# Kernel tuning notes

Hardware: AMD Instinct MI355X
Metric: run time of the kernel (lower is better)

Reference implementation:

```python
import jax, jax.numpy as jnp
import numpy as np
from jax import lax

B = 2048; T = 16; K = 12; G = T * B; NODES = G * (K + 1)
ENC = 64; GIN = 32; GHID = 64; GOUT = 32; EMB = 32; DEMB = 16
DYN = 32; DEC = 128; TOUT = 25; GRID = (13, 3); SCONV = 64; C31 = 16
SOC = ((GRID[0] - 4 + 1) // 2) * C31  # 80
TE = EMB * 3 + DEMB + GOUT            # 144


def _lstm(xs, Wih, Whh, bih, bhh):
    # xs: (T, N, in) seq-first, torch LSTM gate order i,f,g,o
    n = xs.shape[1]; H = Whh.shape[1]
    def step(carry, x):
        h, c = carry
        g = x @ Wih.T + h @ Whh.T + bih + bhh
        i, f, gg, o = jnp.split(g, 4, axis=-1)
        c = jax.nn.sigmoid(f) * c + jax.nn.sigmoid(i) * jnp.tanh(gg)
        h = jax.nn.sigmoid(o) * jnp.tanh(c)
        return (h, c), h
    z = jnp.zeros((n, H), xs.dtype)
    (h, _), hs = lax.scan(step, (z, z), xs)
    return hs, h


def _gat(x, src, dst, W, a_s, a_d, b, n):
    # PyG GATConv, heads=1, self-loops already in src/dst, leaky slope 0.2
    xw = x @ W.T
    e = jax.nn.leaky_relu((xw @ a_s)[src] + (xw @ a_d)[dst], 0.2)
    m = jax.ops.segment_max(e, dst, num_segments=n)
    ex = jnp.exp(e - m[dst])
    den = jax.ops.segment_sum(ex, dst, num_segments=n)
    alpha = ex / den[dst]
    return jax.ops.segment_sum(xw[src] * alpha[:, None], dst, num_segments=n) + b


def setup_inputs() -> dict:
    key = jax.random.key(0)
    ks = iter(jax.random.split(key, 80))
    f = lambda *s: jax.random.normal(next(ks), s, jnp.float32) * 0.05
    base = np.arange(G, dtype=np.int32) * (K + 1)          # ego node of each group
    nb = (base[:, None] + 1 + np.arange(K, dtype=np.int32)).reshape(-1)
    ego = np.repeat(base, K)
    edge_index = jnp.asarray(np.stack([np.concatenate([nb, ego]), np.concatenate([ego, nb])]))
    batch_gat = jnp.asarray(np.repeat(np.arange(G, dtype=np.int32), K + 1))
    m = np.zeros((B, GRID[1] * GRID[0], ENC), bool); m[:, :K, :] = True
    masks = jnp.asarray(m.reshape(B, GRID[1], GRID[0], ENC))
    return dict(
        data_figure_x=f(NODES, 4), edge_index=edge_index, batch_gat=batch_gat,
        hist=f(T, B, 2), hist_va=f(T, B, 2), hist_dis=f(T, B, 1), hist_lane=f(T, B, 2),
        nbrs=f(T, B * K, 2), nbrs_va=f(T, B * K, 2), nbrs_dis=f(T, B * K, 1), nbrs_lane=f(T, B * K, 2),
        masks=masks, lat_enc=f(B, 3), lon_enc=f(B, 2),
        ip_emb_W=f(GIN, 4), ip_emb_b=f(GIN),
        gat1_W=f(GHID, GIN), gat1_as=f(GHID), gat1_ad=f(GHID), gat1_b=f(GHID),
        gat2_W=f(GOUT, GHID), gat2_as=f(GOUT), gat2_ad=f(GOUT), gat2_b=f(GOUT),
        pos_W=f(EMB, 2), pos_b=f(EMB), va_W=f(EMB, 2), va_b=f(EMB),
        dis_W=f(DEMB, 1), dis_b=f(DEMB), lane_W=f(EMB, 2), lane_b=f(EMB),
        enc_Wih=f(4 * ENC, TE), enc_Whh=f(4 * ENC, ENC), enc_bih=f(4 * ENC), enc_bhh=f(4 * ENC),
        ta_Wih=f(4 * ENC, TE), ta_Whh=f(4 * ENC, ENC), ta_bih=f(4 * ENC), ta_bhh=f(4 * ENC),
        ta_TA_W=f(T, T * ENC), ta_TA_b=f(T),
        dyn_W=f(DYN, ENC), dyn_b=f(DYN),
        sconv_W=f(SCONV, ENC, 3, 3), sconv_b=f(SCONV),
        conv31_W=f(C31, SCONV, 3, 1), conv31_b=f(C31),
        dec_Wih=f(4 * DEC, 2 * SOC + DYN + 5), dec_Whh=f(4 * DEC, DEC), dec_bih=f(4 * DEC), dec_bhh=f(4 * DEC),
        op_W=f(5, DEC), op_b=f(5),
        oplat_W=f(3, 2 * SOC + DYN), oplat_b=f(3), oplon_W=f(2, 2 * SOC + DYN), oplon_b=f(2))


def reference(data_figure_x, edge_index, batch_gat, hist, hist_va, hist_dis, hist_lane,
              nbrs, nbrs_va, nbrs_dis, nbrs_lane, masks, lat_enc, lon_enc,
              ip_emb_W, ip_emb_b, gat1_W, gat1_as, gat1_ad, gat1_b,
              gat2_W, gat2_as, gat2_ad, gat2_b,
              pos_W, pos_b, va_W, va_b, dis_W, dis_b, lane_W, lane_b,
              enc_Wih, enc_Whh, enc_bih, enc_bhh,
              ta_Wih, ta_Whh, ta_bih, ta_bhh, ta_TA_W, ta_TA_b,
              dyn_W, dyn_b, sconv_W, sconv_b, conv31_W, conv31_b,
              dec_Wih, dec_Whh, dec_bih, dec_bhh, op_W, op_b,
              oplat_W, oplat_b, oplon_W, oplon_b):
    n = data_figure_x.shape[0]
    lrelu = lambda x: jax.nn.leaky_relu(x, 0.1)
    loop = jnp.arange(n, dtype=edge_index.dtype)
    src = jnp.concatenate([edge_index[0], loop])
    dst = jnp.concatenate([edge_index[1], loop])
    h = lrelu(data_figure_x @ ip_emb_W.T + ip_emb_b)
    h = lrelu(_gat(h, src, dst, gat1_W, gat1_as, gat1_ad, gat1_b, n))
    h = lrelu(_gat(h, src, dst, gat2_W, gat2_as, gat2_ad, gat2_b, n))
    # first node per group -> ego (hist), rest -> neighbors (batch_gat sorted)
    first_idx = jnp.searchsorted(batch_gat, jnp.arange(G, dtype=batch_gat.dtype))
    hist_gat = h[first_idx].reshape(T, B, GOUT)          # dropout = eval identity
    nbr_mask = jnp.ones(n, bool).at[first_idx].set(False)
    nbr_idx = jnp.where(nbr_mask, size=n - G)[0]
    nbrs_gat = h[nbr_idx].reshape(T, -1, GOUT)
    emb = lambda x, W, b: lrelu(x @ W.T + b)
    ch = jnp.concatenate([emb(hist, pos_W, pos_b), emb(hist_va, va_W, va_b),
                          emb(hist_dis, dis_W, dis_b), emb(hist_lane, lane_W, lane_b), hist_gat], -1)
    cn = jnp.concatenate([emb(nbrs, pos_W, pos_b), emb(nbrs_va, va_W, va_b),
                          emb(nbrs_dis, dis_W, dis_b), emb(nbrs_lane, lane_W, lane_b), nbrs_gat], -1)
    # TA_LSTM: temporal attention over per-step hidden states
    hs, _ = _lstm(ch, ta_Wih, ta_Whh, ta_bih, ta_bhh)     # (T, B, ENC)
    total = hs.transpose(1, 0, 2).reshape(B, T * ENC)
    beta = jax.nn.softmax(jax.nn.relu(total @ ta_TA_W.T + ta_TA_b), axis=-1)
    hist_enc = lrelu(jnp.einsum('tbh,bt->bh', hs, beta) @ dyn_W.T + dyn_b)
    _, nbrs_enc = _lstm(cn, enc_Wih, enc_Whh, enc_bih, enc_bhh)   # (B*K, ENC)
    # masked_scatter_: fill True positions row-major with flattened nbrs_enc
    mflat = masks.reshape(-1)
    sidx = jnp.clip(jnp.cumsum(mflat) - 1, 0)
    soc = jnp.where(mflat, nbrs_enc.reshape(-1)[sidx], 0.0).reshape(masks.shape).astype(jnp.float32)
    soc = soc.transpose(0, 3, 2, 1)                       # (B, ENC, 13, 3)
    dn = ('NCHW', 'OIHW', 'NCHW')
    soc = lrelu(lax.conv_general_dilated(soc, sconv_W, (1, 1), 'VALID', dimension_numbers=dn)
                + sconv_b[None, :, None, None])
    soc = lrelu(lax.conv_general_dilated(soc, conv31_W, (1, 1), 'VALID', dimension_numbers=dn)
                + conv31_b[None, :, None, None])          # (B, C31, 9, 1)
    pad = ((0, 0), (0, 0), (1, 1), (0, 0))
    mx = lax.reduce_window(soc, -jnp.inf, lax.max, (1, 1, 2, 1), (1, 1, 2, 1), pad).reshape(-1, SOC)
    av = (lax.reduce_window(soc, 0.0, lax.add, (1, 1, 2, 1), (1, 1, 2, 1), pad) / 2.0).reshape(-1, SOC)
    enc = jnp.concatenate([mx, av, hist_enc], 1)          # (B, 2*SOC+DYN)
    lat_pred = jax.nn.softmax(enc @ oplat_W.T + oplat_b, axis=1)
    lon_pred = jax.nn.softmax(enc @ oplon_W.T + oplon_b, axis=1)
    encd = jnp.concatenate([enc, lat_enc, lon_enc], 1)
    rep = jnp.broadcast_to(encd[None], (TOUT,) + encd.shape)
    hs2, _ = _lstm(rep, dec_Wih, dec_Whh, dec_bih, dec_bhh)
    fut = hs2 @ op_W.T + op_b                             # (TOUT, B, 5)
    out = jnp.concatenate([fut[..., 0:2], jnp.exp(fut[..., 2:4]), jnp.tanh(fut[..., 4:5])], -1)
    return out, lat_pred, lon_pred
```

## Files before the change

### kernel.cpp

```cpp
#include <hip/hip_runtime.h>
#include <hip/hip_bf16.h>
#include <cstddef>
#include <cstdint>
#include <math.h>

typedef __hip_bfloat16 bf16;
typedef _Float16 f16;
typedef _Float16 f16x8 __attribute__((ext_vector_type(8)));
typedef _Float16 f16x2 __attribute__((ext_vector_type(2)));
typedef float f32x4 __attribute__((ext_vector_type(4)));
#define MFMA16(a,b,c) __builtin_amdgcn_mfma_f32_16x16x32_f16(a,b,c,0,0,0)

#define DEV __device__ __forceinline__
DEV float bff(bf16 x){ return __bfloat162float(x); }
DEV bf16 fbf(float x){ return __float2bfloat16(x); }
DEV float lr01(float x){ return x>0.f? x : 0.1f*x; }
DEV float lr02(float x){ return x>0.f? x : 0.2f*x; }
DEV float frcp(float x){ return __builtin_amdgcn_rcpf(x); }
DEV float sigm(float x){ return frcp(1.f+__expf(-x)); }
DEV float tanhe(float x){ float a=fabsf(x); float e=__expf(-2.f*a); float t=(1.f-e)*frcp(1.f+e); return x<0.f? -t : t; }
DEV void stout(void* out, int isf, size_t i, float v){
  if (isf) ((float*)out)[i] = v; else ((bf16*)out)[i] = fbf(v);
}
DEV float bfu_lo(unsigned u){ return __uint_as_float(u << 16); }
DEV float bfu_hi(unsigned u){ return __uint_as_float(u & 0xffff0000u); }

#define NBATCH 2048
#define TSEQ 16
#define KNB 12
#define NGRP 32768
#define NNODES 425984
#define NBK 24576
#define NTOUT 25

__global__ __launch_bounds__(256) void detect_k(const uint32_t* __restrict__ x, int* __restrict__ flag) {
  __shared__ int cnt;
  if (threadIdx.x == 0) cnt = 0;
  __syncthreads();
  float v = __uint_as_float(x[threadIdx.x]);
  float a = fabsf(v);
  if (a > 1e-12f && a < 100.f) atomicAdd(&cnt, 1);
  __syncthreads();
  if (threadIdx.x == 0) *flag = (cnt >= 128) ? 1 : 0;
}

#define NCVT 55
struct CvtArgs {
  const void* src[NCVT];
  unsigned off[NCVT];
  unsigned cnt[NCVT];
};

__global__ __launch_bounds__(256) void cvt_k(CvtArgs a, float* __restrict__ dst,
                                             const int* __restrict__ flag, unsigned total) {
  const int isf = *flag;
  for (size_t e = (size_t)blockIdx.x*256 + threadIdx.x; e < total; e += (size_t)gridDim.x*256) {
    int lo = 0, hi = NCVT-1;
    while (lo < hi) { int mid = (lo+hi+1)>>1; if ((size_t)a.off[mid] <= e) lo = mid; else hi = mid-1; }
    unsigned r = (unsigned)(e - a.off[lo]);
    float v = isf ? ((const float*)a.src[lo])[r] : bff(((const bf16*)a.src[lo])[r]);
    dst[e] = v;
  }
}

__global__ __launch_bounds__(256) void prep_k(
    const float* __restrict__ scW, const float* __restrict__ c31W,
    const float* __restrict__ g1W, const float* __restrict__ g2W,
    const float* __restrict__ encWhh, const float* __restrict__ taWhh,
    const float* __restrict__ decWhh,
    f16* __restrict__ wp1t, f16* __restrict__ wp2t,
    float* __restrict__ w1t, float* __restrict__ w2t,
    f16* __restrict__ wench, f16* __restrict__ wtah, f16* __restrict__ wdech) {
  int idx = blockIdx.x*256 + threadIdx.x;
  if (idx < 12288) {
    int o = idx & 63; int k = idx >> 6; int kh = k >> 6; int i = k & 63;
    wp1t[idx] = (f16)scW[((size_t)(o*64+i)*3 + kh)*3];
  } else if (idx < 15360) {
    int e = idx - 12288;
    int o = e & 15; int k = e >> 4; int kh = k >> 6; int i = k & 63;
    wp2t[e] = (f16)c31W[(size_t)(o*64+i)*3 + kh];
  } else if (idx < 17408) {
    int e = idx - 15360; int k = e >> 6, f = e & 63;
    w1t[e] = g1W[f*32 + k];
  } else if (idx < 19456) {
    int e = idx - 17408; int k = e >> 5, f = e & 31;
    w2t[e] = g2W[f*64 + k];
  } else if (idx < 35840) {
    int e = idx - 19456;
    wench[e] = (f16)encWhh[e];
  } else if (idx < 52224) {
    int e = idx - 35840;
    wtah[e] = (f16)taWhh[e];
  } else if (idx < 117760) {
    int e = idx - 52224;
    wdech[e] = (f16)decWhh[e];
  }
}

__global__ __launch_bounds__(256) void gat_dense1_k(const float* __restrict__ x,
    const float* __restrict__ ipW, const float* __restrict__ ipb,
    const float* __restrict__ Wt, const float* __restrict__ as_, const float* __restrict__ ad_,
    bf16* __restrict__ out, float* __restrict__ esed) {
  __shared__ float As[64][33];
  __shared__ float Ws[32][64];
  __shared__ float xs[64][4];
  __shared__ float wipw[128];
  __shared__ float wipb[32];
  const int tid = threadIdx.x;
  const size_t bm = (size_t)blockIdx.x * 64;
  ((float*)xs)[tid] = x[bm*4 + tid];
  if (tid < 128) wipw[tid] = ipW[tid];
  else if (tid < 160) wipb[tid-128] = ipb[tid-128];
  #pragma unroll
  for (int i = 0; i < 8; i++) ((float*)Ws)[tid + 256*i] = Wt[tid + 256*i];
  __syncthreads();
  #pragma unroll
  for (int i = 0; i < 8; i++) {
    int e = tid + 256*i; int v = e >> 5, f = e & 31;
    float a = wipb[f];
    #pragma unroll
    for (int k = 0; k < 4; k++) a += xs[v][k]*wipw[f*4+k];
    As[v][f] = lr01(a);
  }
  __syncthreads();
  const int v = tid >> 2, f0 = (tid & 3) * 16;
  float acc[16];
  #pragma unroll
  for (int i = 0; i < 16; i++) acc[i] = 0.f;
  #pragma unroll 8
  for (int k = 0; k < 32; k++) {
    float a = As[v][k];
    const float4* wr = (const float4*)&Ws[k][f0];
    #pragma unroll
    for (int q = 0; q < 4; q++) {
      float4 w4 = wr[q];
      acc[4*q+0] += a*w4.x; acc[4*q+1] += a*w4.y; acc[4*q+2] += a*w4.z; acc[4*q+3] += a*w4.w;
    }
  }
  bf16* op = out + (bm+v)*64 + f0;
  #pragma unroll
  for (int i = 0; i < 16; i++) op[i] = fbf(acc[i]);
  float es = 0.f, ed = 0.f;
  #pragma unroll
  for (int i = 0; i < 16; i++) { es += acc[i]*as_[f0+i]; ed += acc[i]*ad_[f0+i]; }
  es += __shfl_xor(es, 1); es += __shfl_xor(es, 2);
  ed += __shfl_xor(ed, 1); ed += __shfl_xor(ed, 2);
  if ((tid & 3) == 0) { esed[(bm+v)*2] = es; esed[(bm+v)*2+1] = ed; }
}

__global__ __launch_bounds__(256) void gat_dense2_k(const bf16* __restrict__ in,
    const float* __restrict__ Wt, const float* __restrict__ as_, const float* __restrict__ ad_,
    bf16* __restrict__ out, float* __restrict__ esed) {
  __shared__ float As[64][65];
  __shared__ float Ws[64][32];
  const int tid = threadIdx.x;
  const size_t bm = (size_t)blockIdx.x * 64;
  #pragma unroll
  for (int i = 0; i < 16; i++) {
    int lin = tid + 256*i;
    As[lin>>6][lin&63] = bff(in[bm*64 + lin]);
    if (i < 8) ((float*)Ws)[tid + 256*i] = Wt[tid + 256*i];
  }
  __syncthreads();
  const int v = tid >> 2, f0 = (tid & 3) * 8;
  float acc[8];
  #pragma unroll
  for (int i = 0; i < 8; i++) acc[i] = 0.f;
  #pragma unroll 8
  for (int k = 0; k < 64; k++) {
    float a = As[v][k];
    const float4* wr = (const float4*)&Ws[k][f0];
    #pragma unroll
    for (int q = 0; q < 2; q++) {
      float4 w4 = wr[q];
      acc[4*q+0] += a*w4.x; acc[4*q+1] += a*w4.y; acc[4*q+2] += a*w4.z; acc[4*q+3] += a*w4.w;
    }
  }
  bf16* op = out + (bm+v)*32 + f0;
  #pragma unroll
  for (int i = 0; i < 8; i++) op[i] = fbf(acc[i]);
  float es = 0.f, ed = 0.f;
  #pragma unroll
  for (int i = 0; i < 8; i++) { es += acc[i]*as_[f0+i]; ed += acc[i]*ad_[f0+i]; }
  es += __shfl_xor(es, 1); es += __shfl_xor(es, 2);
  ed += __shfl_xor(ed, 1); ed += __shfl_xor(ed, 2);
  if ((tid & 3) == 0) { esed[(bm+v)*2] = es; esed[(bm+v)*2+1] = ed; }
}

__global__ __launch_bounds__(256) void alpha_k(const float* __restrict__ esed, float* __restrict__ alph) {
  int g = blockIdx.x*256 + threadIdx.x;
  size_t base = (size_t)g*13;
  float esv[13], edv[13];
  #pragma unroll
  for (int i = 0; i < 13; i++) { esv[i] = esed[(base+i)*2]; edv[i] = esed[(base+i)*2+1]; }
  float* o = alph + (size_t)g*40;
  float e[13]; float m = -1e30f;
  #pragma unroll
  for (int i = 0; i < 13; i++) { float z = lr02(esv[i] + edv[0]); e[i] = z; m = fmaxf(m, z); }
  float den = 0.f;
  #pragma unroll
  for (int i = 0; i < 13; i++) { e[i] = __expf(e[i]-m); den += e[i]; }
  float inv = 1.f/den;
  #pragma unroll
  for (int i = 0; i < 13; i++) o[i] = e[i]*inv;
  #pragma unroll
  for (int j = 1; j <= 12; j++) {
    float z0 = lr02(esv[0] + edv[j]);
    float z1 = lr02(esv[j] + edv[j]);
    float mm = fmaxf(z0, z1);
    float a0 = __expf(z0-mm), a1 = __expf(z1-mm);
    float s = 1.f/(a0+a1);
    o[13 + 2*(j-1)] = a0*s;
    o[14 + 2*(j-1)] = a1*s;
  }
}

template<int F>
__global__ __launch_bounds__(256) void agg8_k(const bf16* __restrict__ xw, const float* __restrict__ alph,
                                              const float* __restrict__ bias, bf16* __restrict__ out) {
  const int NV = F/8;
  size_t idx = (size_t)blockIdx.x*256 + threadIdx.x;
  int f8 = (int)(idx % NV);
  size_t vn = idx / NV;
  int node = (int)(vn % 13);
  size_t g = vn / 13;
  size_t base = g*13;
  const float* al = alph + g*40;
  const int f0 = f8*8;
  float acc[8];
  if (node == 0) {
    #pragma unroll
    for (int j = 0; j < 8; j++) acc[j] = 0.f;
    #pragma unroll
    for (int i = 0; i < 13; i++) {
      const uint4 rv = *(const uint4*)&xw[(base+i)*F + f0];
      float a = al[i];
      acc[0] += a*bfu_lo(rv.x); acc[1] += a*bfu_hi(rv.x);
      acc[2] += a*bfu_lo(rv.y); acc[3] += a*bfu_hi(rv.y);
      acc[4] += a*bfu_lo(rv.z); acc[5] += a*bfu_hi(rv.z);
      acc[6] += a*bfu_lo(rv.w); acc[7] += a*bfu_hi(rv.w);
    }
  } else {
    float a0 = al[13 + 2*(node-1)], a1 = al[14 + 2*(node-1)];
    const uint4 r0v = *(const uint4*)&xw[base*F + f0];
    const uint4 r1v = *(const uint4*)&xw[(base+node)*F + f0];
    acc[0] = a0*bfu_lo(r0v.x) + a1*bfu_lo(r1v.x);
    acc[1] = a0*bfu_hi(r0v.x) + a1*bfu_hi(r1v.x);
    acc[2] = a0*bfu_lo(r0v.y) + a1*bfu_lo(r1v.y);
    acc[3] = a0*bfu_hi(r0v.y) + a1*bfu_hi(r1v.y);
    acc[4] = a0*bfu_lo(r0v.z) + a1*bfu_lo(r1v.z);
    acc[5] = a0*bfu_hi(r0v.z) + a1*bfu_hi(r1v.z);
    acc[6] = a0*bfu_lo(r0v.w) + a1*bfu_lo(r1v.w);
    acc[7] = a0*bfu_hi(r0v.w) + a1*bfu_hi(r1v.w);
  }
  bf16* op = out + vn*F + f0;
  #pragma unroll
  for (int j = 0; j < 8; j++) op[j] = fbf(lr01(acc[j] + bias[f0+j]));
}

template<bool NBR>
__global__ __launch_bounds__(256) void gemm_embed_mfma_k(
    const float* __restrict__ p_in, const float* __restrict__ v_in,
    const float* __restrict__ di_in, const float* __restrict__ l_in,
    const bf16* __restrict__ h2,
    const float* __restrict__ posW, const float* __restrict__ posb,
    const float* __restrict__ vaW, const float* __restrict__ vab,
    const float* __restrict__ disW, const float* __restrict__ disb,
    const float* __restrict__ laneW, const float* __restrict__ laneb,
    const float* __restrict__ W, f16* __restrict__ C, int t0) {
  __shared__ __align__(16) f16 As[128][40];
  __shared__ __align__(16) f16 Bs[128][40];
  const int tid = threadIdx.x;
  const int bm = blockIdx.x * 128, bn = blockIdx.y * 128;
  const int bz = blockIdx.z;
  const int mm = tid & 127, par = tid >> 7;
  int t, n2;
  if (NBR) { t = t0 + bz; n2 = bm + mm; }
  else { int gm = bm + mm; t = gm >> 11; n2 = gm & 2047; }
  const int NROW = NBR ? NBK : NBATCH;
  size_t rn = (size_t)t*NROW + n2;
  const float px0 = p_in[rn*2], px1 = p_in[rn*2+1];
  const float vx0 = v_in[rn*2], vx1 = v_in[rn*2+1];
  const float dx  = di_in[rn];
  const float lx0 = l_in[rn*2], lx1 = l_in[rn*2+1];
  const int b = NBR ? (n2 / KNB) : n2;
  const int node_off = NBR ? (1 + n2 % KNB) : 0;
  const bf16* h2p = h2 + (((size_t)t*NBATCH + b)*13 + node_off)*32;
  const int wn = bn + mm;
  const int l = tid & 63, wv = tid >> 6;
  const int lr = l & 15, lq = l >> 4;
  f32x4 acc[2][8];
  #pragma unroll
  for (int rt = 0; rt < 2; rt++)
    #pragma unroll
    for (int ct = 0; ct < 8; ct++) acc[rt][ct] = (f32x4){0.f,0.f,0.f,0.f};
  for (int ks = 0; ks < 5; ks++) {
    const int k0 = ks*32;
    #pragma unroll
    for (int e = 0; e < 16; e++) {
      int kk = par + 2*e;
      int f = k0 + kk;
      float val;
      if (f < 32) {
        val = lr01(px0*posW[f*2] + px1*posW[f*2+1] + posb[f]);
      } else if (f < 64) {
        int ff = f-32;
        val = lr01(vx0*vaW[ff*2] + vx1*vaW[ff*2+1] + vab[ff]);
      } else if (f < 80) {
        int ff = f-64;
        val = lr01(dx*disW[ff] + disb[ff]);
      } else if (f < 112) {
        int ff = f-80;
        val = lr01(lx0*laneW[ff*2] + lx1*laneW[ff*2+1] + laneb[ff]);
      } else if (f < 144) {
        val = bff(h2p[f-112]);
      } else val = 0.f;
      As[mm][kk] = (f16)val;
      Bs[mm][kk] = (f < 144) ? (f16)W[(size_t)wn*144 + f] : (f16)0.f;
    }
    __syncthreads();
    f16x8 a0 = *(const f16x8*)&As[wv*32 + lr][lq*8];
    f16x8 a1 = *(const f16x8*)&As[wv*32 + 16 + lr][lq*8];
    #pragma unroll
    for (int ct = 0; ct < 8; ct++) {
      f16x8 bfr = *(const f16x8*)&Bs[ct*16 + lr][lq*8];
      acc[0][ct] = MFMA16(a0, bfr, acc[0][ct]);
      acc[1][ct] = MFMA16(a1, bfr, acc[1][ct]);
    }
    __syncthreads();
  }
  #pragma unroll
  for (int rt = 0; rt < 2; rt++)
    #pragma unroll
    for (int ct = 0; ct < 8; ct++)
      #pragma unroll
      for (int rg = 0; rg < 4; rg++) {
        int row = wv*32 + rt*16 + lq*4 + rg;
        int col = ct*16 + lr;
        size_t orow = NBR ? ((size_t)bz*NBK + bm + row) : (size_t)(bm + row);
        C[orow*256 + bn + col] = (f16)acc[rt][ct][rg];
      }
}

__global__ __launch_bounds__(512, 4) void enc_ta_mega_k(
    const float* __restrict__ p_in, const float* __restrict__ v_in,
    const float* __restrict__ di_in, const float* __restrict__ l_in,
    const bf16* __restrict__ h2,
    const float* __restrict__ posW, const float* __restrict__ posb,
    const float* __restrict__ vaW, const float* __restrict__ vab,
    const float* __restrict__ disW, const float* __restrict__ disb,
    const float* __restrict__ laneW, const float* __restrict__ laneb,
    const float* __restrict__ Wih, const f16* __restrict__ Whh16,
    const float* __restrict__ bih, const float* __restrict__ bhh,
    float* __restrict__ hstate,
    const f16* __restrict__ XWta, const f16* __restrict__ Whh16ta,
    const float* __restrict__ bihta, const float* __restrict__ bhhta,
    float* __restrict__ h_all_ta) {
  __shared__ __align__(16) union SMem {
    struct { f16 As_s[2][16][168]; f16 h_s[2][16][72]; float gates[16][258]; } e;
    struct { f16 h_s[16][72]; float gates[16][260]; } a;
  } sm;
  const int tid = threadIdx.x;
  const int l = tid & 63;
  const int lr = l & 15, lq = l >> 4;

  if (blockIdx.x < 128) {
    const int r0 = blockIdx.x * 16;
    const int wv = tid >> 6;
    const int u = l, rg = wv;
    f16x8 bf[4][2];
    if (wv < 4) {
      #pragma unroll
      for (int ct = 0; ct < 4; ct++)
        #pragma unroll
        for (int kt = 0; kt < 2; kt++)
          bf[ct][kt] = *(const f16x8*)&Whh16ta[(size_t)(wv*64 + ct*16 + lr)*64 + kt*32 + lq*8];
    }
    float bj4[4];
    #pragma unroll
    for (int g = 0; g < 4; g++) bj4[g] = bihta[g*64+u] + bhhta[g*64+u];
    for (int i = tid; i < 16*64; i += 512) sm.a.h_s[i>>6][i&63] = (f16)0.f;
    float c[4] = {0.f,0.f,0.f,0.f};
    __syncthreads();
    #pragma unroll 1
    for (int s = 0; s < TSEQ; s++) {
      if (wv < 4) {
        f16x8 a0 = *(const f16x8*)&sm.a.h_s[lr][lq*8];
        f16x8 a1 = *(const f16x8*)&sm.a.h_s[lr][32 + lq*8];
        f32x4 acc[4];
        #pragma unroll
        for (int ct = 0; ct < 4; ct++) {
          acc[ct] = (f32x4){0.f,0.f,0.f,0.f};
          acc[ct] = MFMA16(a0, bf[ct][0], acc[ct]);
          acc[ct] = MFMA16(a1, bf[ct][1], acc[ct]);
        }
        #pragma unroll
        for (int ct = 0; ct < 4; ct++)
          #pragma unroll
          for (int q2 = 0; q2 < 4; q2++)
            sm.a.gates[lq*4 + q2][wv*64 + ct*16 + lr] = acc[ct][q2];
      }
      __syncthreads();
      if (wv < 4) {
        const f16* xwrow = XWta + ((size_t)s*NBATCH + r0)*256;
        #pragma unroll
        for (int q = 0; q < 4; q++) {
          const int r = rg*4 + q;
          float gi = sm.a.gates[r][u]     + bj4[0] + (float)xwrow[(size_t)r*256 + u];
          float gf = sm.a.gates[r][64+u]  + bj4[1] + (float)xwrow[(size_t)r*256 + 64 + u];
          float gg = sm.a.gates[r][128+u] + bj4[2] + (float)xwrow[(size_t)r*256 + 128 + u];
          float go = sm.a.gates[r][192+u] + bj4[3] + (float)xwrow[(size_t)r*256 + 192 + u];
          float cv = sigm(gf)*c[q] + sigm(gi)*tanhe(gg);
          c[q] = cv;
          float hv = sigm(go)*tanhe(cv);
          sm.a.h_s[r][u] = (f16)hv;
          h_all_ta[((size_t)s*NBATCH + r0 + r)*64 + u] = hv;
        }
      }
      __syncthreads();
    }
    return;
  }

  const int r0 = (blockIdx.x - 128) * 16;
  const int w = tid >> 6;
  const int cu0 = w*16 + lr;
  const int cu1 = 128 + cu0;
  f16x8 bxw[2][5];
  f16x8 bhw[2][2];
  float bv[2];
  #pragma unroll
  for (int s = 0; s < 2; s++) {
    const int cu = s ? cu1 : cu0;
    const float* wr = Wih + (size_t)cu*144;
    #pragma unroll
    for (int ks = 0; ks < 5; ks++) {
      f16x8 v;
      #pragma unroll
      for (int j = 0; j < 8; j++) {
        int k = ks*32 + lq*8 + j;
        v[j] = (k < 144) ? (f16)wr[k] : (f16)0.f;
      }
      bxw[s][ks] = v;
    }
    #pragma unroll
    for (int kt = 0; kt < 2; kt++)
      bhw[s][kt] = *(const f16x8*)&Whh16[(size_t)cu*64 + kt*32 + lq*8];
    bv[s] = bih[cu] + bhh[cu];
  }
  const int prow = tid & 15;
  const int pq = tid >> 4;
  const int n2 = r0 + prow;
  const int bb = n2 / KNB;
  const int noff = 1 + n2 - bb*KNB;
  float c0 = 0.f, c1 = 0.f;
  float La = 0.f, Lb = 0.f;
  uint4 HA = {0,0,0,0};
  for (int i = tid; i < 16*64; i += 512) sm.e.h_s[0][i>>6][i&63] = (f16)0.f;

#define ENC_ISSUE(TP) do {                                                   \
    const size_t rnp = (size_t)(TP)*NBK + n2;                                \
    if (pq < 4)       { float2 p = *(const float2*)(p_in + rnp*2); La = p.x; Lb = p.y; } \
    else if (pq < 8)  { float2 p = *(const float2*)(v_in + rnp*2); La = p.x; Lb = p.y; } \
    else if (pq < 10) { La = di_in[rnp]; }                                   \
    else if (pq < 14) { float2 p = *(const float2*)(l_in + rnp*2); La = p.x; Lb = p.y; } \
    else if (pq < 18) { HA = *(const uint4*)(h2 + (((size_t)(TP)*NBATCH + bb)*13 + noff)*32 + (pq-14)*8); } \
  } while (0)

#define ENC_STAGE(BUF) do {                                                  \
    if (pq < 20) {                                                           \
      const int f0 = pq*8;                                                   \
      f16x8 v;                                                               \
      if (f0 < 32) {                                                         \
        _Pragma("unroll")                                                    \
        for (int j = 0; j < 8; j++)                                          \
          v[j] = (f16)lr01(La*posW[(f0+j)*2] + Lb*posW[(f0+j)*2+1] + posb[f0+j]); \
      } else if (f0 < 64) {                                                  \
        _Pragma("unroll")                                                    \
        for (int j = 0; j < 8; j++) {                                        \
          int ff = f0+j-32;                                                  \
          v[j] = (f16)lr01(La*vaW[ff*2] + Lb*vaW[ff*2+1] + vab[ff]);         \
        }                                                                    \
      } else if (f0 < 80) {                                                  \
        _Pragma("unroll")                                                    \
        for (int j = 0; j < 8; j++) {                                        \
          int ff = f0+j-64;                                                  \
          v[j] = (f16)lr01(La*disW[ff] + disb[ff]);                          \
        }                                                                    \
      } else if (f0 < 112) {                                                 \
        _Pragma("unroll")                                                    \
        for (int j = 0; j < 8; j++) {                                        \
          int ff = f0+j-80;                                                  \
          v[j] = (f16)lr01(La*laneW[ff*2] + Lb*laneW[ff*2+1] + laneb[ff]);   \
        }                                                                    \
      } else if (f0 < 144) {                                                 \
        v[0] = (f16)bfu_lo(HA.x); v[1] = (f16)bfu_hi(HA.x);                  \
        v[2] = (f16)bfu_lo(HA.y); v[3] = (f16)bfu_hi(HA.y);                  \
        v[4] = (f16)bfu_lo(HA.z); v[5] = (f16)bfu_hi(HA.z);                  \
        v[6] = (f16)bfu_lo(HA.w); v[7] = (f16)bfu_hi(HA.w);                  \
      } else {                                                               \
        _Pragma("unroll")                                                    \
        for (int j = 0; j < 8; j++) v[j] = (f16)0.f;                         \
      }                                                                      \
      *(f16x8*)&sm.e.As_s[BUF][prow][f0] = v;                                \
    }                                                                        \
  } while (0)

  ENC_ISSUE(0);
  ENC_STAGE(0);
  __syncthreads();
  int cur = 0;
  #pragma unroll 1
  for (int t = 0; t < TSEQ; t++) {
    const int tp = (t+1 < TSEQ) ? t+1 : t;
    ENC_ISSUE(tp);
    {
      f16x8 ae0 = *(const f16x8*)&sm.e.As_s[cur][lr][lq*8];
      f16x8 ae1 = *(const f16x8*)&sm.e.As_s[cur][lr][32 + lq*8];
      f16x8 ae2 = *(const f16x8*)&sm.e.As_s[cur][lr][64 + lq*8];
      f16x8 ae3 = *(const f16x8*)&sm.e.As_s[cur][lr][96 + lq*8];
      f16x8 ae4 = *(const f16x8*)&sm.e.As_s[cur][lr][128 + lq*8];
      f16x8 ah0 = *(const f16x8*)&sm.e.h_s[cur][lr][lq*8];
      f16x8 ah1 = *(const f16x8*)&sm.e.h_s[cur][lr][32 + lq*8];
      #pragma unroll
      for (int s = 0; s < 2; s++) {
        f32x4 a = (f32x4){0.f,0.f,0.f,0.f};
        a = MFMA16(ae0, bxw[s][0], a);
        a = MFMA16(ae1, bxw[s][1], a);
        a = MFMA16(ae2, bxw[s][2], a);
        a = MFMA16(ae3, bxw[s][3], a);
        a = MFMA16(ae4, bxw[s][4], a);
        a = MFMA16(ah0, bhw[s][0], a);
        a = MFMA16(ah1, bhw[s][1], a);
        const int cu = s ? cu1 : cu0;
        #pragma unroll
        for (int q = 0; q < 4; q++)
          sm.e.gates[lq*4 + q][cu] = a[q] + bv[s];
      }
    }
    __syncthreads();
    {
      const int u0 = pq*2;
      const float* gr = &sm.e.gates[prow][0];
      float gi0 = gr[u0],       gi1 = gr[u0+1];
      float gf0 = gr[64+u0],    gf1 = gr[64+u0+1];
      float gg0 = gr[128+u0],   gg1 = gr[128+u0+1];
      float go0 = gr[192+u0],   go1 = gr[192+u0+1];
      float cv0 = sigm(gf0)*c0 + sigm(gi0)*tanhe(gg0);
      float cv1 = sigm(gf1)*c1 + sigm(gi1)*tanhe(gg1);
      c0 = cv0; c1 = cv1;
      f16x2 hv;
      hv[0] = (f16)(sigm(go0)*tanhe(cv0));
      hv[1] = (f16)(sigm(go1)*tanhe(cv1));
      *(f16x2*)&sm.e.h_s[cur^1][prow][u0] = hv;
    }
    ENC_STAGE(cur^1);
    __syncthreads();
    cur ^= 1;
  }
#undef ENC_ISSUE
#undef ENC_STAGE
  for (int i = tid; i < 16*64; i += 512)
    hstate[(size_t)(r0 + (i>>6))*64 + (i&63)] = (float)sm.e.h_s[cur][i>>6][i&63];
}

__global__ __launch_bounds__(256, 2) void gemm_bt(const bf16* __restrict__ A, const float* __restrict__ W,
                                                  float* __restrict__ C, int M, int N, int Kd) {
  __shared__ __align__(16) float As[8][132];
  __shared__ __align__(16) float Bs[8][132];
  const int tid = threadIdx.x;
  const int bm = blockIdx.x * 128, bn = blockIdx.y * 128;
  const int tx = tid & 15, ty = tid >> 4;
  float acc[8][8];
  #pragma unroll
  for (int i = 0; i < 8; i++)
    #pragma unroll
    for (int j = 0; j < 8; j++) acc[i][j] = 0.f;
  for (int k0 = 0; k0 < Kd; k0 += 8) {
    #pragma unroll
    for (int i = 0; i < 4; i++) {
      int lin = tid + 256*i;
      int kk = lin & 7, mm = lin >> 3;
      int gk = k0 + kk;
      As[kk][mm] = (gk < Kd) ? bff(A[(size_t)(bm+mm)*Kd + gk]) : 0.f;
      Bs[kk][mm] = (gk < Kd) ? W[(size_t)(bn+mm)*Kd + gk] : 0.f;
    }
    __syncthreads();
    #pragma unroll
    for (int kk = 0; kk < 8; kk++) {
      float4 a0 = *(const float4*)&As[kk][ty*4];
      float4 a1 = *(const float4*)&As[kk][64+ty*4];
      float4 b0 = *(const float4*)&Bs[kk][tx*4];
      float4 b1 = *(const float4*)&Bs[kk][64+tx*4];
      float av[8] = {a0.x,a0.y,a0.z,a0.w,a1.x,a1.y,a1.z,a1.w};
      float bv[8] = {b0.x,b0.y,b0.z,b0.w,b1.x,b1.y,b1.z,b1.w};
      #pragma unroll
      for (int i = 0; i < 8; i++)
        #pragma unroll
        for (int j = 0; j < 8; j++) acc[i][j] += av[i]*bv[j];
    }
    __syncthreads();
  }
  #pragma unroll
  for (int i = 0; i < 8; i++) {
    int m = bm + (i>>2)*64 + ty*4 + (i&3);
    #pragma unroll
    for (int jh = 0; jh < 2; jh++) {
      float4 v = make_float4(acc[i][jh*4+0], acc[i][jh*4+1], acc[i][jh*4+2], acc[i][jh*4+3]);
      *(float4*)&C[(size_t)m*N + bn + jh*64 + tx*4] = v;
    }
  }
}

__global__ __launch_bounds__(512) void lstm128_mfma_k(const float* __restrict__ XW,
    const f16* __restrict__ Whh16, const float* __restrict__ bih, const float* __restrict__ bhh,
    int steps, float* __restrict__ h_all) {
  __shared__ __align__(16) f16 h_s[2][16][136];
  const int tid = threadIdx.x;
  const int r0 = blockIdx.x * 16;
  const int l = tid & 63, wv = tid >> 6;
  const int lr = l & 15, lq = l >> 4;
  const int u = wv*16 + lr;
  f16x8 bf[4][4];
  #pragma unroll
  for (int g = 0; g < 4; g++)
    #pragma unroll
    for (int kt = 0; kt < 4; kt++)
      bf[g][kt] = *(const f16x8*)&Whh16[(size_t)(g*128 + u)*128 + kt*32 + lq*8];
  float xr[4][4];
  #pragma unroll
  for (int g = 0; g < 4; g++) {
    float bj = bih[g*128 + u] + bhh[g*128 + u];
    #pragma unroll
    for (int rg = 0; rg < 4; rg++)
      xr[g][rg] = XW[(size_t)(r0 + lq*4 + rg)*512 + g*128 + u] + bj;
  }
  for (int i = tid; i < 16*128; i += 512) h_s[0][i>>7][i&127] = (f16)0.f;
  float c[4] = {0.f,0.f,0.f,0.f};
  __syncthreads();
  int cur = 0;
  for (int t = 0; t < steps; t++) {
    f16x8 a0 = *(const f16x8*)&h_s[cur][lr][lq*8];
    f16x8 a1 = *(const f16x8*)&h_s[cur][lr][32 + lq*8];
    f16x8 a2 = *(const f16x8*)&h_s[cur][lr][64 + lq*8];
    f16x8 a3 = *(const f16x8*)&h_s[cur][lr][96 + lq*8];
    f32x4 acc[4];
    #pragma unroll
    for (int g = 0; g < 4; g++) {
      acc[g] = (f32x4){0.f,0.f,0.f,0.f};
      acc[g] = MFMA16(a0, bf[g][0], acc[g]);
      acc[g] = MFMA16(a1, bf[g][1], acc[g]);
      acc[g] = MFMA16(a2, bf[g][2], acc[g]);
      acc[g] = MFMA16(a3, bf[g][3], acc[g]);
    }
    #pragma unroll
    for (int rg = 0; rg < 4; rg++) {
      const int row = lq*4 + rg;
      float gi = acc[0][rg] + xr[0][rg];
      float gf = acc[1][rg] + xr[1][rg];
      float gg = acc[2][rg] + xr[2][rg];
      float go = acc[3][rg] + xr[3][rg];
      float cv = sigm(gf)*c[rg] + sigm(gi)*tanhe(gg);
      c[rg] = cv;
      float hv = sigm(go)*tanhe(cv);
      h_s[cur^1][row][u] = (f16)hv;
      h_all[((size_t)t*NBATCH + r0 + row)*128 + u] = hv;
    }
    __syncthreads();
    cur ^= 1;
  }
}

__global__ __launch_bounds__(256) void ta_fused_k(const float* __restrict__ hs,
    const float* __restrict__ W, const float* __restrict__ bias,
    const float* __restrict__ dynW, const float* __restrict__ dynb,
    float* __restrict__ henc) {
  __shared__ float hsl[8][1024];
  __shared__ float scl[8][16];
  const int tid = threadIdx.x;
  const int b0 = blockIdx.x * 8;
  for (int i = tid; i < 8*1024; i += 256) {
    int bb = i >> 10, r = i & 1023;
    int t = r >> 6, h = r & 63;
    hsl[bb][r] = hs[((size_t)t*NBATCH + b0 + bb)*64 + h];
  }
  __syncthreads();
  if (tid < 128) {
    int bb = tid >> 4, i = tid & 15;
    float acc = bias[i];
    for (int t = 0; t < 16; t++) {
      const float* hr = &hsl[bb][t*64];
      const float* wr = W + (size_t)i*1024 + t*64;
      #pragma unroll
      for (int h = 0; h < 64; h++) acc += hr[h]*wr[h];
    }
    scl[bb][i] = fmaxf(acc, 0.f);
  }
  __syncthreads();
  {
    int bb = tid >> 5, o = tid & 31;
    const float* s = scl[bb];
    float m = s[0];
    #pragma unroll
    for (int t = 1; t < 16; t++) m = fmaxf(m, s[t]);
    float e[16]; float den = 0.f;
    #pragma unroll
    for (int t = 0; t < 16; t++) { e[t] = __expf(s[t]-m); den += e[t]; }
    float inv = 1.f/den;
    float acc = dynb[o];
    for (int t = 0; t < 16; t++) {
      const float* hr = &hsl[bb][t*64];
      float inner = 0.f;
      #pragma unroll
      for (int h = 0; h < 64; h++) inner += hr[h]*dynW[(size_t)o*64 + h];
      acc += (e[t]*inv)*inner;
    }
    henc[(size_t)(b0+bb)*32 + o] = lr01(acc);
  }
}

__global__ __launch_bounds__(256) void fused_conv_k(const float* __restrict__ nenc,
    const f16* __restrict__ wp1t, const f16* __restrict__ wp2t,
    const float* __restrict__ scb, const float* __restrict__ c31b,
    const float* __restrict__ henc, const float* __restrict__ lat_enc, const float* __restrict__ lon_enc,
    float* __restrict__ e192, bf16* __restrict__ encd) {
  __shared__ f16 ws1[12288];
  __shared__ f16 ws2[3072];
  __shared__ float img[4][13][64];
  __shared__ float c1s[4][64][12];
  __shared__ float c2s[4][16][9];
  const int tid = threadIdx.x;
  const int l = tid & 63, wv = tid >> 6;
  const int b = blockIdx.x*4 + wv;
  #pragma unroll
  for (int it = 0; it < 24; it++) ((uint32_t*)ws1)[tid + 256*it] = ((const uint32_t*)wp1t)[tid + 256*it];
  #pragma unroll
  for (int it = 0; it < 6; it++) ((uint32_t*)ws2)[tid + 256*it] = ((const uint32_t*)wp2t)[tid + 256*it];
  #pragma unroll
  for (int it = 0; it < 13; it++)
    img[wv][it][l] = (it < 12) ? nenc[((size_t)b*12 + it)*64 + l] : 0.f;
  __syncthreads();
  {
    const int o = l;
    float acc[11];
    float bv = scb[o];
    #pragma unroll
    for (int h = 0; h < 11; h++) acc[h] = bv;
    for (int k = 0; k < 192; k++) {
      int kh = k >> 6, i = k & 63;
      float w = (float)ws1[k*64 + o];
      const float* ic = img[wv][kh];
      #pragma unroll
      for (int h = 0; h < 11; h++) acc[h] += ic[h*64 + i] * w;
    }
    #pragma unroll
    for (int h = 0; h < 11; h++) c1s[wv][o][h] = lr01(acc[h]);
  }
  __syncthreads();
  if (l < 48) {
    const int o2 = l / 3, jg = l - o2*3;
    float acc[3];
    float bv = c31b[o2];
    #pragma unroll
    for (int m = 0; m < 3; m++) acc[m] = bv;
    for (int k = 0; k < 192; k++) {
      int kh = k >> 6, i = k & 63;
      float w = (float)ws2[k*16 + o2];
      #pragma unroll
      for (int m = 0; m < 3; m++) acc[m] += c1s[wv][i][jg*3 + m + kh] * w;
    }
    #pragma unroll
    for (int m = 0; m < 3; m++) c2s[wv][o2][jg*3 + m] = lr01(acc[m]);
  }
  __syncthreads();
  for (int it = 0; it < 4; it++) {
    int k = l + it*64;
    if (k >= 197) break;
    float val;
    if (k < 192) {
      if (k < 160) {
        bool is_av = (k >= 80);
        int rel = is_av ? (k - 80) : k;
        int o = rel / 5, p = rel - o*5;
        const float* r = c2s[wv][o];
        float v2 = r[2*p];
        if (p == 0) val = is_av ? v2*0.5f : v2;
        else { float v1 = r[2*p-1]; val = is_av ? (v1+v2)*0.5f : fmaxf(v1, v2); }
      } else {
        val = henc[(size_t)b*32 + (k-160)];
      }
      e192[(size_t)b*192 + k] = val;
    } else if (k < 195) {
      val = lat_enc[(size_t)b*3 + (k-192)];
    } else {
      val = lon_enc[(size_t)b*2 + (k-195)];
    }
    encd[(size_t)b*197 + k] = fbf(val);
  }
}

__global__ __launch_bounds__(256) void latlon_k(const float* __restrict__ e192,
    const float* __restrict__ latW, const float* __restrict__ latb,
    const float* __restrict__ lonW, const float* __restrict__ lonb,
    void* __restrict__ out, const int* __restrict__ flag) {
  int b = blockIdx.x*256 + threadIdx.x;
  const int isf = *flag;
  const float* e = e192 + (size_t)b*192;
  float s[3];
  #pragma unroll
  for (int c2 = 0; c2 < 3; c2++) {
    float acc = latb[c2];
    for (int k = 0; k < 192; k++) acc += e[k]*latW[c2*192+k];
    s[c2] = acc;
  }
  float m = fmaxf(s[0], fmaxf(s[1], s[2]));
  float e0 = __expf(s[0]-m), e1 = __expf(s[1]-m), e2 = __expf(s[2]-m);
  float inv = 1.f/(e0+e1+e2);
  stout(out, isf, 256000 + (size_t)b*3 + 0, e0*inv);
  stout(out, isf, 256000 + (size_t)b*3 + 1, e1*inv);
  stout(out, isf, 256000 + (size_t)b*3 + 2, e2*inv);
  float q[2];
  #pragma unroll
  for (int c2 = 0; c2 < 2; c2++) {
    float acc = lonb[c2];
    for (int k = 0; k < 192; k++) acc += e[k]*lonW[c2*192+k];
    q[c2] = acc;
  }
  float m2 = fmaxf(q[0], q[1]);
  float f0 = __expf(q[0]-m2), f1 = __expf(q[1]-m2);
  float inv2 = 1.f/(f0+f1);
  stout(out, isf, 262144 + (size_t)b*2 + 0, f0*inv2);
  stout(out, isf, 262144 + (size_t)b*2 + 1, f1*inv2);
}

__global__ __launch_bounds__(256) void out_k(const float* __restrict__ hs2, const float* __restrict__ opW,
                                             const float* __restrict__ opb,
                                             void* __restrict__ out, const int* __restrict__ flag) {
  int idx = blockIdx.x*256 + threadIdx.x;
  const int isf = *flag;
  const float* h = hs2 + (size_t)idx*128;
  float f[5];
  #pragma unroll
  for (int c2 = 0; c2 < 5; c2++) {
    float acc = opb[c2];
    #pragma unroll
    for (int k = 0; k < 128; k++) acc += h[k]*opW[c2*128+k];
    f[c2] = acc;
  }
  stout(out, isf, (size_t)idx*5 + 0, f[0]);
  stout(out, isf, (size_t)idx*5 + 1, f[1]);
  stout(out, isf, (size_t)idx*5 + 2, __expf(f[2]));
  stout(out, isf, (size_t)idx*5 + 3, __expf(f[3]));
  stout(out, isf, (size_t)idx*5 + 4, tanhe(f[4]));
}

static const size_t OFF_H2   = 0;
static const size_t OFF_P    = 6815744;
static const size_t OFF_Q    = 20447232;
static const size_t OFF_ESED = 34078720;
static const size_t OFF_ALPH = 34930688;
static const size_t OFF_XWTA = 6815744;
static const size_t OFF_HSTA = 15204352;
static const size_t OFF_SCO  = 17301504;
static const size_t OFF_HS2  = 6815744;
static const size_t OFF_HST  = 23691264;
static const size_t OFF_CST  = 25264128;
static const size_t OFF_E192 = 28573696;
static const size_t OFF_ENCD = 28966912;
static const size_t OFF_XWD  = 29168640;
static const size_t OFF_HEN  = 35000000;
static const size_t OFF_CVT  = 36241408;
static const size_t OFF_WP1T = 41280000;
static const size_t OFF_WP2T = 41286144;
static const size_t OFF_W1T  = 41287680;
static const size_t OFF_W2T  = 41289728;
static const size_t OFF_WENC = 41291776;
static const size_t OFF_WTAH = 41299968;
static const size_t OFF_WDECH= 41308160;
static const size_t OFF_FLAG = 41400000;

extern "C" void kernel_launch(void* const* d_in, const int* in_sizes, int n_in,
                              void* d_out, int out_size, void* d_ws, size_t ws_size,
                              hipStream_t stream) {
  (void)in_sizes; (void)n_in; (void)out_size; (void)ws_size;
  float* ws = (float*)d_ws;
  int* flag = (int*)(ws + OFF_FLAG);

  static const int   cidx[NCVT] = {0,3,4,5,6,7,8,9,10,12,13,
    14,15,16,17,18,19,20,21,22,23,24,25,26,27,28,29,30,31,
    32,33,34,35,36,37,38,39,40,41,42,43,44,45,46,47,
    48,49,50,51,52,53,54,55,56,57};
  static const unsigned ccnt[NCVT] = {1703936,65536,65536,32768,65536,786432,786432,393216,786432,6144,4096,
    128,32,2048,64,64,64,2048,32,32,32,64,32,64,32,16,16,64,32,
    36864,16384,256,256,36864,16384,256,256,16384,16,2048,32,36864,64,3072,16,
    100864,65536,512,512,640,5,576,3,384,2};
  CvtArgs ca;
  unsigned total = 0;
  float* cp[58];
  for (int i = 0; i < NCVT; i++) {
    ca.src[i] = d_in[cidx[i]];
    ca.off[i] = total;
    ca.cnt[i] = ccnt[i];
    cp[cidx[i]] = ws + OFF_CVT + total;
    total += ccnt[i];
  }
  detect_k<<<1,256,0,stream>>>((const uint32_t*)d_in[0], flag);
  cvt_k<<<4096,256,0,stream>>>(ca, ws + OFF_CVT, flag, total);

  void* out = d_out;
  bf16*  h2    = (bf16*)(ws + OFF_H2);
  bf16*  h1    = (bf16*)(ws + OFF_P);
  bf16*  xw1   = (bf16*)(ws + OFF_Q);
  bf16*  xw2   = (bf16*)(ws + OFF_Q);
  float* esed  = ws + OFF_ESED;
  float* alph  = ws + OFF_ALPH;
  f16*   xwta  = (f16*)(ws + OFF_XWTA);
  float* hsta  = ws + OFF_HSTA;
  float* henc  = ws + OFF_HEN;
  float* hst   = ws + OFF_HST;
  float* e192  = ws + OFF_E192;
  bf16*  encd  = (bf16*)(ws + OFF_ENCD);
  float* xwd   = ws + OFF_XWD;
  f16*   wp1t  = (f16*)(ws + OFF_WP1T);
  f16*   wp2t  = (f16*)(ws + OFF_WP2T);
  float* w1t   = ws + OFF_W1T;
  float* w2t   = ws + OFF_W2T;
  f16*   wench = (f16*)(ws + OFF_WENC);
  f16*   wtah  = (f16*)(ws + OFF_WTAH);
  f16*   wdech = (f16*)(ws + OFF_WDECH);
  float* hs2   = ws + OFF_HS2;

  prep_k<<<460,256,0,stream>>>(cp[44], cp[46], cp[16], cp[20], cp[33], cp[37], cp[49],
                               wp1t, wp2t, w1t, w2t, wench, wtah, wdech);

  gat_dense1_k<<<6656,256,0,stream>>>(cp[0], cp[14], cp[15], w1t, cp[17], cp[18], xw1, esed);
  alpha_k<<<128,256,0,stream>>>(esed, alph);
  agg8_k<64><<<13312,256,0,stream>>>(xw1, alph, cp[19], h1);
  gat_dense2_k<<<6656,256,0,stream>>>(h1, w2t, cp[21], cp[22], xw2, esed);
  alpha_k<<<128,256,0,stream>>>(esed, alph);
  agg8_k<32><<<6656,256,0,stream>>>(xw2, alph, cp[23], h2);

  gemm_embed_mfma_k<false><<<dim3(256,2,1),256,0,stream>>>(cp[3], cp[4], cp[5], cp[6], h2,
      cp[24],cp[25],cp[26],cp[27],cp[28],cp[29],cp[30],cp[31], cp[36], xwta, 0);

  enc_ta_mega_k<<<1664,512,0,stream>>>(cp[7], cp[8], cp[9], cp[10], h2,
      cp[24],cp[25],cp[26],cp[27],cp[28],cp[29],cp[30],cp[31],
      cp[32], wench, cp[34], cp[35], hst,
      xwta, wtah, cp[38], cp[39], hsta);

  ta_fused_k<<<256,256,0,stream>>>(hsta, cp[40], cp[41], cp[42], cp[43], henc);

  fused_conv_k<<<512,256,0,stream>>>(hst, wp1t, wp2t, cp[45], cp[47], henc, cp[12], cp[13], e192, encd);

  latlon_k<<<8,256,0,stream>>>(e192, cp[54], cp[55], cp[56], cp[57], out, flag);
  gemm_bt<<<dim3(16,4),256,0,stream>>>(encd, cp[48], xwd, NBATCH, 512, 197);
  lstm128_mfma_k<<<128,512,0,stream>>>(xwd, wdech, cp[50], cp[51], NTOUT, hs2);
  out_k<<<200,256,0,stream>>>(hs2, cp[52], cp[53], out, flag);
}
```

Measured before the change: 737.7 us.

## Fuse latlon head into decoder GEMM and output projection into decoder LSTM

Merges the lat/lon softmax kernel into the decoder input GEMM launch, with extra blocks handling the heads. It also folds the 5-wide output projection into the decoder LSTM loop, using an fp32 shared-memory copy of h instead of writing the full hidden history to global memory. This removes two kernel launches and the hs2 round trip to global memory. The cost is 80 threads doing a serial 128-length dot product each step inside the recurrent loop, which lengthens the critical path per step.

```diff
diff --git a/kernel.cpp b/kernel.cpp
--- a/kernel.cpp
+++ b/kernel.cpp
@@ -564,63 +564,103 @@
     hstate[(size_t)(r0 + (i>>6))*64 + (i&63)] = (float)sm.e.h_s[cur][i>>6][i&63];
 }
 
-__global__ __launch_bounds__(256, 2) void gemm_bt(const bf16* __restrict__ A, const float* __restrict__ W,
-                                                  float* __restrict__ C, int M, int N, int Kd) {
-  __shared__ __align__(16) float As[8][132];
-  __shared__ __align__(16) float Bs[8][132];
+__global__ __launch_bounds__(256, 2) void head_k(const bf16* __restrict__ A, const float* __restrict__ W,
+    float* __restrict__ C, int N, int Kd,
+    const float* __restrict__ e192,
+    const float* __restrict__ latW, const float* __restrict__ latb,
+    const float* __restrict__ lonW, const float* __restrict__ lonb,
+    void* __restrict__ out, const int* __restrict__ flag) {
   const int tid = threadIdx.x;
-  const int bm = blockIdx.x * 128, bn = blockIdx.y * 128;
-  const int tx = tid & 15, ty = tid >> 4;
-  float acc[8][8];
-  #pragma unroll
-  for (int i = 0; i < 8; i++)
-    #pragma unroll
-    for (int j = 0; j < 8; j++) acc[i][j] = 0.f;
-  for (int k0 = 0; k0 < Kd; k0 += 8) {
-    #pragma unroll
-    for (int i = 0; i < 4; i++) {
-      int lin = tid + 256*i;
-      int kk = lin & 7, mm = lin >> 3;
-      int gk = k0 + kk;
-      As[kk][mm] = (gk < Kd) ? bff(A[(size_t)(bm+mm)*Kd + gk]) : 0.f;
-      Bs[kk][mm] = (gk < Kd) ? W[(size_t)(bn+mm)*Kd + gk] : 0.f;
-    }
-    __syncthreads();
-    #pragma unroll
-    for (int kk = 0; kk < 8; kk++) {
-      float4 a0 = *(const float4*)&As[kk][ty*4];
-      float4 a1 = *(const float4*)&As[kk][64+ty*4];
-      float4 b0 = *(const float4*)&Bs[kk][tx*4];
-      float4 b1 = *(const float4*)&Bs[kk][64+tx*4];
-      float av[8] = {a0.x,a0.y,a0.z,a0.w,a1.x,a1.y,a1.z,a1.w};
-      float bv[8] = {b0.x,b0.y,b0.z,b0.w,b1.x,b1.y,b1.z,b1.w};
-      #pragma unroll
-      for (int i = 0; i < 8; i++)
+  if (blockIdx.x < 64) {
+    __shared__ __align__(16) float As[8][132];
+    __shared__ __align__(16) float Bs[8][132];
+    const int bm = (blockIdx.x >> 2) * 128, bn = (blockIdx.x & 3) * 128;
+    const int tx = tid & 15, ty = tid >> 4;
+    float acc[8][8];
+    #pragma unroll
+    for (int i = 0; i < 8; i++)
+      #pragma unroll
+      for (int j = 0; j < 8; j++) acc[i][j] = 0.f;
+    for (int k0 = 0; k0 < Kd; k0 += 8) {
+      #pragma unroll
+      for (int i = 0; i < 4; i++) {
+        int lin = tid + 256*i;
+        int kk = lin & 7, mm = lin >> 3;
+        int gk = k0 + kk;
+        As[kk][mm] = (gk < Kd) ? bff(A[(size_t)(bm+mm)*Kd + gk]) : 0.f;
+        Bs[kk][mm] = (gk < Kd) ? W[(size_t)(bn+mm)*Kd + gk] : 0.f;
+      }
+      __syncthreads();
+      #pragma unroll
+      for (int kk = 0; kk < 8; kk++) {
+        float4 a0 = *(const float4*)&As[kk][ty*4];
+        float4 a1 = *(const float4*)&As[kk][64+ty*4];
+        float4 b0 = *(const float4*)&Bs[kk][tx*4];
+        float4 b1 = *(const float4*)&Bs[kk][64+tx*4];
+        float av[8] = {a0.x,a0.y,a0.z,a0.w,a1.x,a1.y,a1.z,a1.w};
+        float bvv[8] = {b0.x,b0.y,b0.z,b0.w,b1.x,b1.y,b1.z,b1.w};
         #pragma unroll
-        for (int j = 0; j < 8; j++) acc[i][j] += av[i]*bv[j];
-    }
-    __syncthreads();
-  }
-  #pragma unroll
-  for (int i = 0; i < 8; i++) {
-    int m = bm + (i>>2)*64 + ty*4 + (i&3);
-    #pragma unroll
-    for (int jh = 0; jh < 2; jh++) {
-      float4 v = make_float4(acc[i][jh*4+0], acc[i][jh*4+1], acc[i][jh*4+2], acc[i][jh*4+3]);
-      *(float4*)&C[(size_t)m*N + bn + jh*64 + tx*4] = v;
-    }
-  }
-}
-
-__global__ __launch_bounds__(512) void lstm128_mfma_k(const float* __restrict__ XW,
+        for (int i = 0; i < 8; i++)
+          #pragma unroll
+          for (int j = 0; j < 8; j++) acc[i][j] += av[i]*bvv[j];
+      }
+      __syncthreads();
+    }
+    #pragma unroll
+    for (int i = 0; i < 8; i++) {
+      int m = bm + (i>>2)*64 + ty*4 + (i&3);
+      #pragma unroll
+      for (int jh = 0; jh < 2; jh++) {
+        float4 v = make_float4(acc[i][jh*4+0], acc[i][jh*4+1], acc[i][jh*4+2], acc[i][jh*4+3]);
+        *(float4*)&C[(size_t)m*N + bn + jh*64 + tx*4] = v;
+      }
+    }
+  } else {
+    int b = (blockIdx.x - 64)*256 + tid;
+    const int isf = *flag;
+    const float* e = e192 + (size_t)b*192;
+    float s[3];
+    #pragma unroll
+    for (int c2 = 0; c2 < 3; c2++) {
+      float acc = latb[c2];
+      for (int k = 0; k < 192; k++) acc += e[k]*latW[c2*192+k];
+      s[c2] = acc;
+    }
+    float m = fmaxf(s[0], fmaxf(s[1], s[2]));
+    float e0 = __expf(s[0]-m), e1 = __expf(s[1]-m), e2 = __expf(s[2]-m);
+    float inv = 1.f/(e0+e1+e2);
+    stout(out, isf, 256000 + (size_t)b*3 + 0, e0*inv);
+    stout(out, isf, 256000 + (size_t)b*3 + 1, e1*inv);
+    stout(out, isf, 256000 + (size_t)b*3 + 2, e2*inv);
+    float q[2];
+    #pragma unroll
+    for (int c2 = 0; c2 < 2; c2++) {
+      float acc = lonb[c2];
+      for (int k = 0; k < 192; k++) acc += e[k]*lonW[c2*192+k];
+      q[c2] = acc;
+    }
+    float m2 = fmaxf(q[0], q[1]);
+    float f0 = __expf(q[0]-m2), f1 = __expf(q[1]-m2);
+    float inv2 = 1.f/(f0+f1);
+    stout(out, isf, 262144 + (size_t)b*2 + 0, f0*inv2);
+    stout(out, isf, 262144 + (size_t)b*2 + 1, f1*inv2);
+  }
+}
+
+__global__ __launch_bounds__(512) void lstm128_out_k(const float* __restrict__ XW,
     const f16* __restrict__ Whh16, const float* __restrict__ bih, const float* __restrict__ bhh,
-    int steps, float* __restrict__ h_all) {
+    int steps, const float* __restrict__ opW, const float* __restrict__ opb,
+    void* __restrict__ out, const int* __restrict__ flag) {
   __shared__ __align__(16) f16 h_s[2][16][136];
+  __shared__ float hsf[2][16][132];
+  __shared__ float opWs[640];
+  __shared__ float opbs[5];
   const int tid = threadIdx.x;
   const int r0 = blockIdx.x * 16;
   const int l = tid & 63, wv = tid >> 6;
   const int lr = l & 15, lq = l >> 4;
   const int u = wv*16 + lr;
+  const int isf = *flag;
   f16x8 bf[4][4];
   #pragma unroll
   for (int g = 0; g < 4; g++)
@@ -636,9 +676,12 @@
       xr[g][rg] = XW[(size_t)(r0 + lq*4 + rg)*512 + g*128 + u] + bj;
   }
   for (int i = tid; i < 16*128; i += 512) h_s[0][i>>7][i&127] = (f16)0.f;
+  for (int i = tid; i < 640; i += 512) opWs[i] = opW[i];
+  if (tid < 5) opbs[tid] = opb[tid];
   float c[4] = {0.f,0.f,0.f,0.f};
   __syncthreads();
   int cur = 0;
+  #pragma unroll 1
   for (int t = 0; t < steps; t++) {
     f16x8 a0 = *(const f16x8*)&h_s[cur][lr][lq*8];
     f16x8 a1 = *(const f16x8*)&h_s[cur][lr][32 + lq*8];
@@ -664,9 +707,18 @@
       c[rg] = cv;
       float hv = sigm(go)*tanhe(cv);
       h_s[cur^1][row][u] = (f16)hv;
-      h_all[((size_t)t*NBATCH + r0 + row)*128 + u] = hv;
+      hsf[cur^1][row][u] = hv;
     }
     __syncthreads();
+    if (tid < 80) {
+      const int row = tid / 5, c2 = tid - (tid/5)*5;
+      float acc2 = opbs[c2];
+      const float* hr = &hsf[cur^1][row][0];
+      for (int k = 0; k < 128; k++) acc2 += hr[k]*opWs[c2*128+k];
+      size_t oidx = ((size_t)t*NBATCH + r0 + row)*5 + c2;
+      float v = (c2 < 2) ? acc2 : (c2 < 4 ? __expf(acc2) : tanhe(acc2));
+      stout(out, isf, oidx, v);
+    }
     cur ^= 1;
   }
 }
@@ -797,61 +849,6 @@
     }
     encd[(size_t)b*197 + k] = fbf(val);
   }
-}
-
-__global__ __launch_bounds__(256) void latlon_k(const float* __restrict__ e192,
-    const float* __restrict__ latW, const float* __restrict__ latb,
-    const float* __restrict__ lonW, const float* __restrict__ lonb,
-    void* __restrict__ out, const int* __restrict__ flag) {
-  int b = blockIdx.x*256 + threadIdx.x;
-  const int isf = *flag;
-  const float* e = e192 + (size_t)b*192;
-  float s[3];
-  #pragma unroll
-  for (int c2 = 0; c2 < 3; c2++) {
-    float acc = latb[c2];
-    for (int k = 0; k < 192; k++) acc += e[k]*latW[c2*192+k];
-    s[c2] = acc;
-  }
-  float m = fmaxf(s[0], fmaxf(s[1], s[2]));
-  float e0 = __expf(s[0]-m), e1 = __expf(s[1]-m), e2 = __expf(s[2]-m);
-  float inv = 1.f/(e0+e1+e2);
-  stout(out, isf, 256000 + (size_t)b*3 + 0, e0*inv);
-  stout(out, isf, 256000 + (size_t)b*3 + 1, e1*inv);
-  stout(out, isf, 256000 + (size_t)b*3 + 2, e2*inv);
-  float q[2];
-  #pragma unroll
-  for (int c2 = 0; c2 < 2; c2++) {
-    float acc = lonb[c2];
-    for (int k = 0; k < 192; k++) acc += e[k]*lonW[c2*192+k];
-    q[c2] = acc;
-  }
-  float m2 = fmaxf(q[0], q[1]);
-  float f0 = __expf(q[0]-m2), f1 = __expf(q[1]-m2);
-  float inv2 = 1.f/(f0+f1);
-  stout(out, isf, 262144 + (size_t)b*2 + 0, f0*inv2);
-  stout(out, isf, 262144 + (size_t)b*2 + 1, f1*inv2);
-}
-
-__global__ __launch_bounds__(256) void out_k(const float* __restrict__ hs2, const float* __restrict__ opW,
-                                             const float* __restrict__ opb,
-                                             void* __restrict__ out, const int* __restrict__ flag) {
-  int idx = blockIdx.x*256 + threadIdx.x;
-  const int isf = *flag;
-  const float* h = hs2 + (size_t)idx*128;
-  float f[5];
-  #pragma unroll
-  for (int c2 = 0; c2 < 5; c2++) {
-    float acc = opb[c2];
-    #pragma unroll
-    for (int k = 0; k < 128; k++) acc += h[k]*opW[c2*128+k];
-    f[c2] = acc;
-  }
-  stout(out, isf, (size_t)idx*5 + 0, f[0]);
-  stout(out, isf, (size_t)idx*5 + 1, f[1]);
-  stout(out, isf, (size_t)idx*5 + 2, __expf(f[2]));
-  stout(out, isf, (size_t)idx*5 + 3, __expf(f[3]));
-  stout(out, isf, (size_t)idx*5 + 4, tanhe(f[4]));
 }
 
 static const size_t OFF_H2   = 0;
@@ -928,7 +925,6 @@
   f16*   wench = (f16*)(ws + OFF_WENC);
   f16*   wtah  = (f16*)(ws + OFF_WTAH);
   f16*   wdech = (f16*)(ws + OFF_WDECH);
-  float* hs2   = ws + OFF_HS2;
 
   prep_k<<<460,256,0,stream>>>(cp[44], cp[46], cp[16], cp[20], cp[33], cp[37], cp[49],
                                wp1t, wp2t, w1t, w2t, wench, wtah, wdech);
@@ -952,8 +948,9 @@
 
   fused_conv_k<<<512,256,0,stream>>>(hst, wp1t, wp2t, cp[45], cp[47], henc, cp[12], cp[13], e192, encd);
 
-  latlon_k<<<8,256,0,stream>>>(e192, cp[54], cp[55], cp[56], cp[57], out, flag);
-  gemm_bt<<<dim3(16,4),256,0,stream>>>(encd, cp[48], xwd, NBATCH, 512, 197);
-  lstm128_mfma_k<<<128,512,0,stream>>>(xwd, wdech, cp[50], cp[51], NTOUT, hs2);
-  out_k<<<200,256,0,stream>>>(hs2, cp[52], cp[53], out, flag);
-}
+  head_k<<<72,256,0,stream>>>(encd, cp[48], xwd, 512, 197,
+      e192, cp[54], cp[55], cp[56], cp[57], out, flag);
+
+  lstm128_out_k<<<128,512,0,stream>>>(xwd, wdech, cp[50], cp[51], NTOUT,
+      cp[52], cp[53], out, flag);
+}
```

Result: faster. 717.0 us (-2.8%).
